# Optimization experiments

Measured on AMD Instinct MI355X. Metric: run time of the kernel, lower is better.

Reference implementation:

```python
import jax, jax.numpy as jnp
import numpy as np

# Model dims
E, K, D, F = 8, 2, 1024, 2048   # num_experts, top_k, d_model, d_ff
B, S = 2, 1024                  # batch, seq -> T = 2048 tokens


def setup_inputs() -> dict:
    key = jax.random.key(0)
    k1, k2, k3, k4 = jax.random.split(key, 4)
    hidden = jax.random.normal(k1, (B, S, D), dtype=jnp.float32)
    gate_logits = jax.random.normal(k2, (B * S, E), dtype=jnp.float32)
    # Expert FFN params: expert_e(x) = silu(x @ W1[e]) @ W2[e]
    W1 = jax.random.normal(k3, (E, D, F), dtype=jnp.float32) * 0.02
    W2 = jax.random.normal(k4, (E, F, D), dtype=jnp.float32) * 0.02
    return {"hidden": hidden, "gate_logits": gate_logits, "W1": W1, "W2": W2}


def reference(hidden, gate_logits, W1, W2):
    b, s, d = hidden.shape
    x = hidden.reshape(-1, d)                                  # [T, D]
    # Router: softmax -> top-k -> renormalize (gate_logits path of forward)
    probs = jax.nn.softmax(gate_logits, axis=-1)               # [T, E]
    topk_w, topk_idx = jax.lax.top_k(probs, K)                 # [T, K]
    topk_w = topk_w / jnp.sum(topk_w, axis=-1, keepdims=True)
    # Combine weights as a dense [T, E] map (top_k indices are distinct)
    tok_w = jnp.sum(jax.nn.one_hot(topk_idx, E, dtype=topk_w.dtype)
                    * topk_w[..., None], axis=1)               # [T, E]
    # Grouped expert FFN, expressed densely over the expert axis; the
    # combine weights zero out non-selected experts, so the math equals the
    # original gather -> per-expert GEMM -> weighted scatter-combine.
    h = jax.nn.silu(jnp.einsum('td,edf->tef', x, W1))          # [T, E, F]
    y = jnp.einsum('tef,efd->ted', h, W2)                      # [T, E, D]
    out = jnp.einsum('te,ted->td', tok_w, y)                   # [T, D]
    return out.reshape(b, s, d)
```

## Files before the change

### kernel.cpp

```cpp
#include <hip/hip_runtime.h>
#include <hip/hip_bf16.h>

#define E_N 8
#define D_DIM 1024
#define F_DIM 2048
#define T_N 2048
#define NSLOT 4096

typedef unsigned short u16;
typedef unsigned int u32;
typedef unsigned long long u64;
typedef float floatx4 __attribute__((ext_vector_type(4)));
typedef short bf16x8v __attribute__((ext_vector_type(8)));

__device__ __forceinline__ u16 f2bf(float f) {
    union { float f; u32 u; } v; v.f = f;
    u32 r = v.u + 0x7FFFu + ((v.u >> 16) & 1u);
    return (u16)(r >> 16);
}

__device__ __forceinline__ void gll16(const void* g, void* l) {
    __builtin_amdgcn_global_load_lds((const __attribute__((address_space(1))) void*)g,
                                     (__attribute__((address_space(3))) void*)l, 16, 0, 0);
}

__global__ void router_kernel(const float* __restrict__ gl,
                              int* __restrict__ cnt, int* __restrict__ base,
                              int* __restrict__ slot_tok, float* __restrict__ slot_w) {
    __shared__ int scnt[E_N];
    __shared__ int sbase[E_N];
    const int tid = threadIdx.x;
    if (tid < E_N) scnt[tid] = 0;
    __syncthreads();
    int e0a[8], e1a[8], p0a[8], p1a[8];
    float w0a[8];
#pragma unroll
    for (int i = 0; i < 8; ++i) {
        const int t = tid + i * 256;
        const float4* gp = (const float4*)(gl + (size_t)t * E_N);
        const float4 x0 = gp[0], x1 = gp[1];
        float l[E_N] = {x0.x, x0.y, x0.z, x0.w, x1.x, x1.y, x1.z, x1.w};
        int e0 = 0; float m0 = l[0];
#pragma unroll
        for (int e = 1; e < E_N; ++e) if (l[e] > m0) { m0 = l[e]; e0 = e; }
        int e1 = -1; float m1 = -1e30f;
#pragma unroll
        for (int e = 0; e < E_N; ++e) if (e != e0 && l[e] > m1) { m1 = l[e]; e1 = e; }
        const float p = __expf(m1 - m0);
        w0a[i] = 1.0f / (1.0f + p);
        e0a[i] = e0; e1a[i] = e1;
        p0a[i] = atomicAdd(&scnt[e0], 1);
        p1a[i] = atomicAdd(&scnt[e1], 1);
    }
    __syncthreads();
    if (tid == 0) {
        int s = 0;
        for (int e = 0; e < E_N; ++e) { sbase[e] = s; base[e] = s; cnt[e] = scnt[e]; s += scnt[e]; }
    }
    __syncthreads();
#pragma unroll
    for (int i = 0; i < 8; ++i) {
        const int t = tid + i * 256;
        const int s0 = sbase[e0a[i]] + p0a[i];
        const int s1 = sbase[e1a[i]] + p1a[i];
        slot_tok[s0] = t; slot_tok[s1] = t;
        slot_w[s0] = w0a[i]; slot_w[s1] = 1.0f - w0a[i];
    }
}

__device__ __forceinline__ void cvt_tile(const float* __restrict__ src, u16* __restrict__ dst,
                                         int R, int C, int tr, int tc, int e, char* LT) {
    const int r0 = tr << 6, c0 = tc << 6;
    const int t = threadIdx.x;
    const int rowq = t >> 4, col4 = t & 15;
    const float* sp = src + (size_t)e * R * C + (size_t)(r0 + rowq * 4) * C + c0 + col4 * 4;
    float4 v[4];
#pragma unroll
    for (int i = 0; i < 4; ++i) v[i] = *(const float4*)(sp + (size_t)i * C);
    const float* f = (const float*)v;
#pragma unroll
    for (int j = 0; j < 4; ++j) {
        const int c = col4 * 4 + j;
        u64 pk = (u64)f2bf(f[0 * 4 + j]) | ((u64)f2bf(f[1 * 4 + j]) << 16)
               | ((u64)f2bf(f[2 * 4 + j]) << 32) | ((u64)f2bf(f[3 * 4 + j]) << 48);
        *(u64*)(LT + c * 144 + ((rowq ^ col4) << 3)) = pk;
    }
    __syncthreads();
    u16* dp = dst + (size_t)e * R * C;
#pragma unroll
    for (int i = 0; i < 2; ++i) {
        const int id = i * 256 + t;
        const int c = id >> 3, seg = id & 7;
        const int x = (c >> 2) & 15;
        const u64 lo = *(const u64*)(LT + c * 144 + (((2 * seg) ^ x) << 3));
        const u64 hi = *(const u64*)(LT + c * 144 + (((2 * seg + 1) ^ x) << 3));
        u64 q[2] = {lo, hi};
        *(uint4*)(dp + (size_t)(c0 + c) * R + r0 + seg * 8) = *(const uint4*)q;
    }
}

__global__ __launch_bounds__(256) void prep_kernel(const float* __restrict__ W1,
                                                   const float* __restrict__ W2,
                                                   const float* __restrict__ X,
                                                   const int* __restrict__ slot_tok,
                                                   u16* __restrict__ W1T, u16* __restrict__ W2T,
                                                   u16* __restrict__ Xg) {
    __shared__ __align__(16) char LT[64 * 144];
    const int b = blockIdx.x;
    if (b < 4096) {
        const int e = b >> 9, rem = b & 511;
        cvt_tile(W1, W1T, D_DIM, F_DIM, rem >> 5, rem & 31, e, LT);
    } else if (b < 8192) {
        const int e = (b - 4096) >> 9, rem = (b - 4096) & 511;
        cvt_tile(W2, W2T, F_DIM, D_DIM, rem >> 4, rem & 15, e, LT);
    } else {
        const int g = b - 8192;
        const int t = threadIdx.x;
        const int s = 4 * g + (t >> 6), lane = t & 63;
        const int tok = slot_tok[s];
        const float* xp = X + (size_t)tok * D_DIM + lane * 4;
        u16* gp = Xg + (size_t)s * D_DIM + lane * 4;
#pragma unroll
        for (int p = 0; p < 4; ++p) {
            const float4 v = *(const float4*)(xp + p * 256);
            union { u16 o[4]; uint2 q; } u;
            u.o[0] = f2bf(v.x); u.o[1] = f2bf(v.y); u.o[2] = f2bf(v.z); u.o[3] = f2bf(v.w);
            *(uint2*)(gp + p * 256) = u.q;
        }
    }
}

template<bool G1>
__global__ __launch_bounds__(256) void moe_gemm_kernel(
        const u16* __restrict__ A, const u16* __restrict__ B,
        const int* __restrict__ cnt, const int* __restrict__ basep,
        const int* __restrict__ slot_tok, const float* __restrict__ slot_w,
        u16* __restrict__ hout, float* __restrict__ out) {
    constexpr int KA = G1 ? D_DIM : F_DIM;
    constexpr int KB = KA;
    constexpr int KIT = 16;
    const int e  = G1 ? blockIdx.z : (blockIdx.z >> 1);
    const int kh = G1 ? 0 : (blockIdx.z & 1);
    const int mt = blockIdx.y;
    const int nt = blockIdx.x;
    const int cnt_e = cnt[e];
    if (mt * 128 >= cnt_e) return;
    const int m0 = basep[e] + mt * 128;
    const int vm = cnt_e - mt * 128;

    __shared__ __align__(16) u16 Alds[8192];
    __shared__ __align__(16) u16 Blds[8192];

    const int tid = threadIdx.x;
    const int wid = tid >> 6, lane = tid & 63;
    const int l3 = lane >> 3, l7 = lane & 7;
    const int stgRow = wid * 8 + l3;
    const int stgCol = ((l7 ^ l3) << 3);

    const u16* aS = A + (size_t)(m0 + stgRow) * KA + kh * (F_DIM / 2) + stgCol;
    const u16* bS = B + (size_t)e * ((size_t)D_DIM * F_DIM)
                      + (size_t)(nt * 128 + stgRow) * KB + kh * (F_DIM / 2) + stgCol;

    const int wm = (wid >> 1) * 64, wn = (wid & 1) * 64;
    const int lr = lane & 15, lq = lane >> 4;
    const int aoff = (wm + lr) * 64;
    const int boff = (wn + lr) * 64;
    const int sw0 = ((lq)     ^ l7) << 3;
    const int sw1 = ((lq + 4) ^ l7) << 3;

    floatx4 acc[4][4];
    const floatx4 zero = {0.f, 0.f, 0.f, 0.f};
#pragma unroll
    for (int i = 0; i < 4; ++i)
#pragma unroll
        for (int j = 0; j < 4; ++j) acc[i][j] = zero;

    for (int kt = 0; kt < KIT; ++kt) {
#pragma unroll
        for (int c = 0; c < 4; ++c) {
            gll16(aS + (size_t)(c * 32) * KA, &Alds[c * 2048 + wid * 512]);
            gll16(bS + (size_t)(c * 32) * KB, &Blds[c * 2048 + wid * 512]);
        }
        aS += 64; bS += 64;
        __syncthreads();
#pragma unroll
        for (int ks = 0; ks < 2; ++ks) {
            const int sw = ks ? sw1 : sw0;
            bf16x8v af[4], bfv[4];
#pragma unroll
            for (int mi = 0; mi < 4; ++mi) af[mi]  = *(const bf16x8v*)&Alds[aoff + mi * 1024 + sw];
#pragma unroll
            for (int ni = 0; ni < 4; ++ni) bfv[ni] = *(const bf16x8v*)&Blds[boff + ni * 1024 + sw];
#pragma unroll
            for (int mi = 0; mi < 4; ++mi)
#pragma unroll
                for (int ni = 0; ni < 4; ++ni)
                    acc[mi][ni] = __builtin_amdgcn_mfma_f32_16x16x32_bf16(af[mi], bfv[ni], acc[mi][ni], 0, 0, 0);
        }
        __syncthreads();
    }

    if constexpr (G1) {
#pragma unroll
        for (int mi = 0; mi < 4; ++mi)
#pragma unroll
            for (int r = 0; r < 4; ++r) {
                const int rl = wm + mi * 16 + lq * 4 + r;
                if (rl < vm) {
                    const float w = slot_w[m0 + rl];
                    u16* hp = hout + (size_t)(m0 + rl) * F_DIM + nt * 128 + wn + lr;
#pragma unroll
                    for (int ni = 0; ni < 4; ++ni) {
                        const float v = acc[mi][ni][r];
                        hp[ni * 16] = f2bf(w * v / (1.0f + __expf(-v)));
                    }
                }
            }
    } else {
#pragma unroll
        for (int mi = 0; mi < 4; ++mi)
#pragma unroll
            for (int r = 0; r < 4; ++r) {
                const int rl = wm + mi * 16 + lq * 4 + r;
                if (rl < vm) {
                    const int tok = slot_tok[m0 + rl];
                    float* op = out + (size_t)tok * D_DIM + nt * 128 + wn + lr;
#pragma unroll
                    for (int ni = 0; ni < 4; ++ni) atomicAdd(&op[ni * 16], acc[mi][ni][r]);
                }
            }
    }
}

extern "C" void kernel_launch(void* const* d_in, const int* in_sizes, int n_in,
                              void* d_out, int out_size, void* d_ws, size_t ws_size,
                              hipStream_t stream) {
    const float* hidden = (const float*)d_in[0];
    const float* gl     = (const float*)d_in[1];
    const float* W1     = (const float*)d_in[2];
    const float* W2     = (const float*)d_in[3];
    float* out = (float*)d_out;

    char* ws = (char*)d_ws;
    int* m = (int*)ws;
    int* cnt      = m;
    int* basep    = m + 16;
    int* slot_tok = m + 32;
    float* slot_w = (float*)(m + 32 + 4096);

    const size_t HBYTES  = (size_t)(NSLOT + 128) * F_DIM * 2;
    const size_t W1BYTES = (size_t)E_N * D_DIM * F_DIM * 2;
    const size_t XBYTES  = (size_t)(NSLOT + 128) * D_DIM * 2;
    u16* h   = (u16*)(ws + (1 << 16));
    u16* W1T = (u16*)(ws + (1 << 16) + HBYTES);
    u16* Xg  = (u16*)(ws + (1 << 16) + HBYTES + W1BYTES);
    u16* W2T = (u16*)(ws + (1 << 16) + HBYTES + W1BYTES + XBYTES);

    hipMemsetAsync(d_out, 0, (size_t)out_size * sizeof(float), stream);
    router_kernel<<<1, 256, 0, stream>>>(gl, cnt, basep, slot_tok, slot_w);
    prep_kernel<<<8192 + NSLOT / 4, 256, 0, stream>>>(W1, W2, hidden, slot_tok, W1T, W2T, Xg);
    moe_gemm_kernel<true><<<dim3(F_DIM / 128, 16, E_N), 256, 0, stream>>>(
        Xg, W1T, cnt, basep, slot_tok, slot_w, h, nullptr);
    moe_gemm_kernel<false><<<dim3(D_DIM / 128, 16, E_N * 2), 256, 0, stream>>>(
        h, W2T, cnt, basep, slot_tok, slot_w, nullptr, out);
}
```

Measured before the change: 266.7 us.

## Parallelize router, fold slot scatter and output zeroing into prep kernel

The router now runs on 8 blocks with per-block expert counts, and the prefix-sum and slot assignment move into the prep kernel. Each token block there computes its slot offsets and writes the bf16 activations to both expert slots. The separate hipMemsetAsync of the output is replaced by extra zeroing blocks inside prep. The weight-transpose blocks each handle two 64-column tiles, halving the block count, which lowers launch overhead and the serial single-block router latency at the cost of redundant count summation per block.

```diff
diff --git a/kernel.cpp b/kernel.cpp
--- a/kernel.cpp
+++ b/kernel.cpp
@@ -24,109 +24,150 @@
                                      (__attribute__((address_space(3))) void*)l, 16, 0, 0);
 }
 
-__global__ void router_kernel(const float* __restrict__ gl,
-                              int* __restrict__ cnt, int* __restrict__ base,
-                              int* __restrict__ slot_tok, float* __restrict__ slot_w) {
+__global__ __launch_bounds__(256) void router_kernel(const float* __restrict__ gl,
+                                                     int4* __restrict__ tok_meta,
+                                                     float* __restrict__ tok_w0,
+                                                     int* __restrict__ bcnt) {
     __shared__ int scnt[E_N];
-    __shared__ int sbase[E_N];
-    const int tid = threadIdx.x;
+    const int tid = threadIdx.x, b = blockIdx.x;
     if (tid < E_N) scnt[tid] = 0;
     __syncthreads();
-    int e0a[8], e1a[8], p0a[8], p1a[8];
-    float w0a[8];
-#pragma unroll
-    for (int i = 0; i < 8; ++i) {
-        const int t = tid + i * 256;
-        const float4* gp = (const float4*)(gl + (size_t)t * E_N);
-        const float4 x0 = gp[0], x1 = gp[1];
-        float l[E_N] = {x0.x, x0.y, x0.z, x0.w, x1.x, x1.y, x1.z, x1.w};
-        int e0 = 0; float m0 = l[0];
-#pragma unroll
-        for (int e = 1; e < E_N; ++e) if (l[e] > m0) { m0 = l[e]; e0 = e; }
-        int e1 = -1; float m1 = -1e30f;
-#pragma unroll
-        for (int e = 0; e < E_N; ++e) if (e != e0 && l[e] > m1) { m1 = l[e]; e1 = e; }
-        const float p = __expf(m1 - m0);
-        w0a[i] = 1.0f / (1.0f + p);
-        e0a[i] = e0; e1a[i] = e1;
-        p0a[i] = atomicAdd(&scnt[e0], 1);
-        p1a[i] = atomicAdd(&scnt[e1], 1);
-    }
+    const int t = b * 256 + tid;
+    const float4* gp = (const float4*)(gl + (size_t)t * E_N);
+    const float4 x0 = gp[0], x1 = gp[1];
+    float l[E_N] = {x0.x, x0.y, x0.z, x0.w, x1.x, x1.y, x1.z, x1.w};
+    int e0 = 0; float m0 = l[0];
+#pragma unroll
+    for (int e = 1; e < E_N; ++e) if (l[e] > m0) { m0 = l[e]; e0 = e; }
+    int e1 = -1; float m1 = -1e30f;
+#pragma unroll
+    for (int e = 0; e < E_N; ++e) if (e != e0 && l[e] > m1) { m1 = l[e]; e1 = e; }
+    const float p = __expf(m1 - m0);
+    const float w0 = 1.0f / (1.0f + p);
+    const int r0 = atomicAdd(&scnt[e0], 1);
+    const int r1 = atomicAdd(&scnt[e1], 1);
+    tok_meta[t] = make_int4(e0, e1, r0, r1);
+    tok_w0[t] = w0;
     __syncthreads();
-    if (tid == 0) {
-        int s = 0;
-        for (int e = 0; e < E_N; ++e) { sbase[e] = s; base[e] = s; cnt[e] = scnt[e]; s += scnt[e]; }
-    }
-    __syncthreads();
-#pragma unroll
-    for (int i = 0; i < 8; ++i) {
-        const int t = tid + i * 256;
-        const int s0 = sbase[e0a[i]] + p0a[i];
-        const int s1 = sbase[e1a[i]] + p1a[i];
-        slot_tok[s0] = t; slot_tok[s1] = t;
-        slot_w[s0] = w0a[i]; slot_w[s1] = 1.0f - w0a[i];
-    }
-}
-
-__device__ __forceinline__ void cvt_tile(const float* __restrict__ src, u16* __restrict__ dst,
-                                         int R, int C, int tr, int tc, int e, char* LT) {
-    const int r0 = tr << 6, c0 = tc << 6;
+    if (tid < E_N) bcnt[b * E_N + tid] = scnt[tid];
+}
+
+__device__ __forceinline__ void cvt_pair(const float* __restrict__ src, u16* __restrict__ dst,
+                                         int R, int C, int tr, int tcp, int e, char* LT) {
+    const int r0 = tr << 6, c0 = tcp << 7;
     const int t = threadIdx.x;
     const int rowq = t >> 4, col4 = t & 15;
     const float* sp = src + (size_t)e * R * C + (size_t)(r0 + rowq * 4) * C + c0 + col4 * 4;
-    float4 v[4];
-#pragma unroll
-    for (int i = 0; i < 4; ++i) v[i] = *(const float4*)(sp + (size_t)i * C);
-    const float* f = (const float*)v;
+    float4 v0[4], v1[4];
+#pragma unroll
+    for (int i = 0; i < 4; ++i) v0[i] = *(const float4*)(sp + (size_t)i * C);
+#pragma unroll
+    for (int i = 0; i < 4; ++i) v1[i] = *(const float4*)(sp + (size_t)i * C + 64);
+    u16* dp = dst + (size_t)e * R * C;
+
+    const float* f0 = (const float*)v0;
 #pragma unroll
     for (int j = 0; j < 4; ++j) {
         const int c = col4 * 4 + j;
-        u64 pk = (u64)f2bf(f[0 * 4 + j]) | ((u64)f2bf(f[1 * 4 + j]) << 16)
-               | ((u64)f2bf(f[2 * 4 + j]) << 32) | ((u64)f2bf(f[3 * 4 + j]) << 48);
+        u64 pk = (u64)f2bf(f0[0 * 4 + j]) | ((u64)f2bf(f0[1 * 4 + j]) << 16)
+               | ((u64)f2bf(f0[2 * 4 + j]) << 32) | ((u64)f2bf(f0[3 * 4 + j]) << 48);
         *(u64*)(LT + c * 144 + ((rowq ^ col4) << 3)) = pk;
     }
     __syncthreads();
-    u16* dp = dst + (size_t)e * R * C;
 #pragma unroll
     for (int i = 0; i < 2; ++i) {
         const int id = i * 256 + t;
         const int c = id >> 3, seg = id & 7;
         const int x = (c >> 2) & 15;
-        const u64 lo = *(const u64*)(LT + c * 144 + (((2 * seg) ^ x) << 3));
-        const u64 hi = *(const u64*)(LT + c * 144 + (((2 * seg + 1) ^ x) << 3));
-        u64 q[2] = {lo, hi};
+        u64 q[2];
+        q[0] = *(const u64*)(LT + c * 144 + (((2 * seg) ^ x) << 3));
+        q[1] = *(const u64*)(LT + c * 144 + (((2 * seg + 1) ^ x) << 3));
         *(uint4*)(dp + (size_t)(c0 + c) * R + r0 + seg * 8) = *(const uint4*)q;
     }
-}
-
-__global__ __launch_bounds__(256) void prep_kernel(const float* __restrict__ W1,
-                                                   const float* __restrict__ W2,
-                                                   const float* __restrict__ X,
-                                                   const int* __restrict__ slot_tok,
-                                                   u16* __restrict__ W1T, u16* __restrict__ W2T,
-                                                   u16* __restrict__ Xg) {
-    __shared__ __align__(16) char LT[64 * 144];
+    const float* f1 = (const float*)v1;
+#pragma unroll
+    for (int j = 0; j < 4; ++j) {
+        const int c = col4 * 4 + j;
+        u64 pk = (u64)f2bf(f1[0 * 4 + j]) | ((u64)f2bf(f1[1 * 4 + j]) << 16)
+               | ((u64)f2bf(f1[2 * 4 + j]) << 32) | ((u64)f2bf(f1[3 * 4 + j]) << 48);
+        *(u64*)(LT + 9216 + c * 144 + ((rowq ^ col4) << 3)) = pk;
+    }
+    __syncthreads();
+#pragma unroll
+    for (int i = 0; i < 2; ++i) {
+        const int id = i * 256 + t;
+        const int c = id >> 3, seg = id & 7;
+        const int x = (c >> 2) & 15;
+        u64 q[2];
+        q[0] = *(const u64*)(LT + 9216 + c * 144 + (((2 * seg) ^ x) << 3));
+        q[1] = *(const u64*)(LT + 9216 + c * 144 + (((2 * seg + 1) ^ x) << 3));
+        *(uint4*)(dp + (size_t)(c0 + 64 + c) * R + r0 + seg * 8) = *(const uint4*)q;
+    }
+}
+
+__global__ __launch_bounds__(256) void prep_kernel(
+        const float* __restrict__ W1, const float* __restrict__ W2,
+        const float* __restrict__ X, float* __restrict__ out,
+        const int4* __restrict__ tok_meta, const float* __restrict__ tok_w0,
+        const int* __restrict__ bcnt,
+        int* __restrict__ cnt, int* __restrict__ basep,
+        int* __restrict__ slot_tok, float* __restrict__ slot_w,
+        u16* __restrict__ W1T, u16* __restrict__ W2T, u16* __restrict__ Xg) {
+    __shared__ __align__(16) char LT[18432];
+    __shared__ int sb[64];
     const int b = blockIdx.x;
-    if (b < 4096) {
-        const int e = b >> 9, rem = b & 511;
-        cvt_tile(W1, W1T, D_DIM, F_DIM, rem >> 5, rem & 31, e, LT);
-    } else if (b < 8192) {
-        const int e = (b - 4096) >> 9, rem = (b - 4096) & 511;
-        cvt_tile(W2, W2T, F_DIM, D_DIM, rem >> 4, rem & 15, e, LT);
-    } else {
-        const int g = b - 8192;
-        const int t = threadIdx.x;
-        const int s = 4 * g + (t >> 6), lane = t & 63;
-        const int tok = slot_tok[s];
-        const float* xp = X + (size_t)tok * D_DIM + lane * 4;
-        u16* gp = Xg + (size_t)s * D_DIM + lane * 4;
+    const int tid = threadIdx.x;
+    if (b < 2048) {
+        const int e = b >> 8, p = b & 255;
+        cvt_pair(W1, W1T, D_DIM, F_DIM, p >> 4, p & 15, e, LT);
+    } else if (b < 4096) {
+        const int b2 = b - 2048;
+        const int e = b2 >> 8, p = b2 & 255;
+        cvt_pair(W2, W2T, F_DIM, D_DIM, p >> 3, p & 7, e, LT);
+    } else if (b < 4608) {
+        const int g = b - 4096;
+        if (tid < 64) sb[tid] = bcnt[tid];
+        __syncthreads();
+        int cntE[E_N], baseE[E_N];
+        {
+            int s = 0;
+#pragma unroll
+            for (int e = 0; e < E_N; ++e) {
+                int c = 0;
+#pragma unroll
+                for (int k = 0; k < 8; ++k) c += sb[k * E_N + e];
+                cntE[e] = c; baseE[e] = s; s += c;
+            }
+        }
+        const int t = g * 4 + (tid >> 6), lane = tid & 63;
+        const int4 mt = tok_meta[t];
+        const float w0 = tok_w0[t];
+        const int bt = t >> 8;
+        int o0 = baseE[mt.x], o1 = baseE[mt.y];
+        for (int k = 0; k < bt; ++k) { o0 += sb[k * E_N + mt.x]; o1 += sb[k * E_N + mt.y]; }
+        const int s0 = o0 + mt.z, s1 = o1 + mt.w;
+        const float* xp = X + (size_t)t * D_DIM + lane * 4;
+        u16* g0 = Xg + (size_t)s0 * D_DIM + lane * 4;
+        u16* g1 = Xg + (size_t)s1 * D_DIM + lane * 4;
 #pragma unroll
         for (int p = 0; p < 4; ++p) {
             const float4 v = *(const float4*)(xp + p * 256);
             union { u16 o[4]; uint2 q; } u;
             u.o[0] = f2bf(v.x); u.o[1] = f2bf(v.y); u.o[2] = f2bf(v.z); u.o[3] = f2bf(v.w);
-            *(uint2*)(gp + p * 256) = u.q;
-        }
+            *(uint2*)(g0 + p * 256) = u.q;
+            *(uint2*)(g1 + p * 256) = u.q;
+        }
+        if (lane == 0) {
+            slot_tok[s0] = t; slot_tok[s1] = t;
+            slot_w[s0] = w0; slot_w[s1] = 1.0f - w0;
+        }
+        if (g == 0 && tid < E_N) { cnt[tid] = cntE[tid]; basep[tid] = baseE[tid]; }
+    } else {
+        const int z = b - 4608;
+        float4 zq = {0.f, 0.f, 0.f, 0.f};
+        float* op = out + (size_t)z * 2048 + tid * 8;
+        *(float4*)op = zq;
+        *(float4*)(op + 4) = zq;
     }
 }
 
@@ -242,23 +283,26 @@
     float* out = (float*)d_out;
 
     char* ws = (char*)d_ws;
-    int* m = (int*)ws;
-    int* cnt      = m;
-    int* basep    = m + 16;
-    int* slot_tok = m + 32;
-    float* slot_w = (float*)(m + 32 + 4096);
-
+    int*   cnt      = (int*)(ws + 0);
+    int*   basep    = (int*)(ws + 64);
+    int*   bcnt     = (int*)(ws + 128);
+    int4*  tok_meta = (int4*)(ws + 512);
+    float* tok_w0   = (float*)(ws + 512 + 32768);
+    int*   slot_tok = (int*)(ws + 512 + 40960);
+    float* slot_w   = (float*)(ws + 512 + 57344);
+
+    const size_t META    = 131072;
     const size_t HBYTES  = (size_t)(NSLOT + 128) * F_DIM * 2;
     const size_t W1BYTES = (size_t)E_N * D_DIM * F_DIM * 2;
     const size_t XBYTES  = (size_t)(NSLOT + 128) * D_DIM * 2;
-    u16* h   = (u16*)(ws + (1 << 16));
-    u16* W1T = (u16*)(ws + (1 << 16) + HBYTES);
-    u16* Xg  = (u16*)(ws + (1 << 16) + HBYTES + W1BYTES);
-    u16* W2T = (u16*)(ws + (1 << 16) + HBYTES + W1BYTES + XBYTES);
-
-    hipMemsetAsync(d_out, 0, (size_t)out_size * sizeof(float), stream);
-    router_kernel<<<1, 256, 0, stream>>>(gl, cnt, basep, slot_tok, slot_w);
-    prep_kernel<<<8192 + NSLOT / 4, 256, 0, stream>>>(W1, W2, hidden, slot_tok, W1T, W2T, Xg);
+    u16* h   = (u16*)(ws + META);
+    u16* W1T = (u16*)(ws + META + HBYTES);
+    u16* Xg  = (u16*)(ws + META + HBYTES + W1BYTES);
+    u16* W2T = (u16*)(ws + META + HBYTES + W1BYTES + XBYTES);
+
+    router_kernel<<<8, 256, 0, stream>>>(gl, tok_meta, tok_w0, bcnt);
+    prep_kernel<<<5632, 256, 0, stream>>>(W1, W2, hidden, out, tok_meta, tok_w0, bcnt,
+                                          cnt, basep, slot_tok, slot_w, W1T, W2T, Xg);
     moe_gemm_kernel<true><<<dim3(F_DIM / 128, 16, E_N), 256, 0, stream>>>(
         Xg, W1T, cnt, basep, slot_tok, slot_w, h, nullptr);
     moe_gemm_kernel<false><<<dim3(D_DIM / 128, 16, E_N * 2), 256, 0, stream>>>(
```

Result: faster. 258.9 us (-2.9%).
